# Performance work log

Measured on AMD Instinct MI355X. Metric: run time of the kernel, lower is better.

## Reference

```python
import jax, jax.numpy as jnp
import numpy as np

B_, C_, K_, STRIDE, HH = 32, 32, 3, 2, 16
H_ = 4   # h = sqrt(hh)
W_SP = 14  # input spatial width w
BATCH = 4


def setup_inputs() -> dict:
    key = jax.random.key(0)
    k1, k2, k3, k4 = jax.random.split(key, 4)
    poses = jax.random.normal(k1, (BATCH, C_, W_SP, W_SP, HH), jnp.float32)
    # variance strictly positive to keep sqrt well-behaved
    var = jax.random.uniform(k2, (BATCH, 1, C_ * W_SP * W_SP, HH), jnp.float32) * 0.9 + 0.1
    Wt = jax.random.normal(k3, (B_, K_, K_, C_, H_, H_), jnp.float32)
    # fixed gaussian noise for the reparameterized torch.normal(mu, sigma)
    noise = jax.random.normal(k4, (BATCH, B_ * K_ * K_, C_ * W_SP * W_SP, HH), jnp.float32)
    return {"poses": poses, "var": var, "Wt": Wt, "noise": noise, "out_hw": 29}


def reference(poses, var, Wt, noise, out_hw):
    b, C, w = poses.shape[0], poses.shape[1], poses.shape[2]
    Bc, K, _, _, h, _ = Wt.shape
    hh = h * h
    # inverse_EM: votes ~ Normal(mu, sqrt(var)), reparameterized
    mu = poses.reshape(b, 1, C * w * w, hh)                    # (b,1,Cww,hh)
    votes = mu + jnp.sqrt(var) * noise                          # (b,B*K*K,Cww,hh)
    # spatial flatten order of Cww is (c, j, i): k = j*w + i in the fold loop
    votes = votes.reshape(b, Bc, K, K, C, w, w, h, h)           # (b,B,ki,kj,c,j,i,h,h)
    # W_hat @ votes, then .sum over C -- fused into one einsum
    v = jnp.einsum("nklcuv,bnklcjivw->bnkljiuw", Wt, votes)     # (b,B,ki,kj,j,i,h,h)
    v = v.reshape(b, Bc, K, K, w, w, hh)                        # (b,B,ki,kj,j,i,hh)
    # fold / col2im: recon[:, :, s*i+ki, s*j+kj, :] += v[:, :, ki, kj, j, i, :]
    upd = v.transpose(0, 1, 2, 5, 3, 4, 6)                      # (b,B,ki,i,kj,j,hh)
    offs = STRIDE * jnp.arange(w)[None, :] + jnp.arange(K)[:, None]  # (K,w)
    rows = offs[:, :, None, None]                               # (K,w,1,1) -> ki,i
    cols = offs[None, None, :, :]                               # (1,1,K,w) -> kj,j
    recon = jnp.zeros((b, Bc, out_hw, out_hw, hh), poses.dtype)
    recon = recon.at[:, :, rows, cols, :].add(upd)
    return recon
```

## Files before the change

kernel.cpp:

```cpp
#include <hip/hip_runtime.h>
#include <math.h>


#define N_KL 288
#define CW2  6272
#define SPATIAL 196

__global__ void sqrt_var_kernel(const float* __restrict__ var,
                                float* __restrict__ sd, int n) {
  int idx = blockIdx.x * blockDim.x + threadIdx.x;
  if (idx < n) sd[idx] = sqrtf(var[idx]);
}

__global__ __launch_bounds__(256) void convcaps_phase1(
    const float* __restrict__ mu,
    const float* __restrict__ sd,
    const float* __restrict__ Wt,
    const float* __restrict__ noise,
    float* __restrict__ upd)
{
  __shared__ float wlds[1024];
  const int tid = threadIdx.x;
  const int BN = N_KL * SPATIAL;

  const long long S0 = (long long)blockIdx.x * 64;
  const int b0   = (int)(S0 / BN);
  const int rem0 = (int)(S0 - (long long)b0 * BN);
  const int nkl0 = rem0 / SPATIAL;
  const int nkl1 = (rem0 + 63) / SPATIAL;

  for (int f = tid; f < 1024; f += 256) {
    int sel = f >> 9;
    int rem = f & 511;
    int c = rem >> 4;
    int u = (rem >> 2) & 3;
    int v = rem & 3;
    int nk = sel ? nkl1 : nkl0;
    wlds[sel * 512 + c * 16 + v * 4 + u] = Wt[nk * 512 + rem];
  }
  __syncthreads();

  const int site_local = tid >> 2;
  const int v = tid & 3;
  const int rem = rem0 + site_local;
  const int nkl = rem / SPATIAL;
  const int s = rem - nkl * SPATIAL;
  const int sel = (nkl != nkl0) ? 1 : 0;

  const float* __restrict__ nb =
      noise + ((size_t)(b0 * N_KL + nkl) * CW2 + s) * 16 + v * 4;
  const float* __restrict__ mb = mu + ((size_t)b0 * CW2 + s) * 16 + v * 4;
  const float* __restrict__ sb = sd + ((size_t)b0 * CW2 + s) * 16 + v * 4;
  const float4* __restrict__ wf4 = (const float4*)wlds + sel * 128 + v;

  float4 acc0 = {0.f,0.f,0.f,0.f}, acc1 = {0.f,0.f,0.f,0.f};
  float4 acc2 = {0.f,0.f,0.f,0.f}, acc3 = {0.f,0.f,0.f,0.f};

  #pragma unroll 4
  for (int c = 0; c < 32; ++c) {
    const size_t off = (size_t)c * (SPATIAL * 16);
    float4 nz = *(const float4*)(nb + off);
    float4 m  = *(const float4*)(mb + off);
    float4 sv = *(const float4*)(sb + off);
    float4 w  = wf4[c * 4];
    float4 vt;
    vt.x = fmaf(sv.x, nz.x, m.x);
    vt.y = fmaf(sv.y, nz.y, m.y);
    vt.z = fmaf(sv.z, nz.z, m.z);
    vt.w = fmaf(sv.w, nz.w, m.w);
    acc0.x = fmaf(w.x, vt.x, acc0.x); acc0.y = fmaf(w.x, vt.y, acc0.y);
    acc0.z = fmaf(w.x, vt.z, acc0.z); acc0.w = fmaf(w.x, vt.w, acc0.w);
    acc1.x = fmaf(w.y, vt.x, acc1.x); acc1.y = fmaf(w.y, vt.y, acc1.y);
    acc1.z = fmaf(w.y, vt.z, acc1.z); acc1.w = fmaf(w.y, vt.w, acc1.w);
    acc2.x = fmaf(w.z, vt.x, acc2.x); acc2.y = fmaf(w.z, vt.y, acc2.y);
    acc2.z = fmaf(w.z, vt.z, acc2.z); acc2.w = fmaf(w.z, vt.w, acc2.w);
    acc3.x = fmaf(w.w, vt.x, acc3.x); acc3.y = fmaf(w.w, vt.y, acc3.y);
    acc3.z = fmaf(w.w, vt.z, acc3.z); acc3.w = fmaf(w.w, vt.w, acc3.w);
  }

  #define QRED(a) \
    a.x += __shfl_xor(a.x, 1); a.y += __shfl_xor(a.y, 1); \
    a.z += __shfl_xor(a.z, 1); a.w += __shfl_xor(a.w, 1); \
    a.x += __shfl_xor(a.x, 2); a.y += __shfl_xor(a.y, 2); \
    a.z += __shfl_xor(a.z, 2); a.w += __shfl_xor(a.w, 2);
  QRED(acc0) QRED(acc1) QRED(acc2) QRED(acc3)
  #undef QRED

  float4 r01 = (v & 1) ? acc1 : acc0;
  float4 r23 = (v & 1) ? acc3 : acc2;
  float4 myrow = (v & 2) ? r23 : r01;
  *(float4*)(upd + (S0 + site_local) * 16 + v * 4) = myrow;
}

__global__ __launch_bounds__(256) void convcaps_phase2(
    const float* __restrict__ upd, float* __restrict__ out, int total4)
{
  int t = blockIdx.x * 256 + threadIdx.x;
  if (t >= total4) return;
  int q = t & 3;
  int p = t >> 2;
  int cc = p % 29; p /= 29;
  int r  = p % 29; p /= 29;
  int n  = p & 31;
  int b  = p >> 5;

  float4 acc = {0.f, 0.f, 0.f, 0.f};
  #pragma unroll
  for (int k = 0; k < 3; ++k) {
    int ri = r - k;
    if (ri < 0 || (ri & 1)) continue;
    int i = ri >> 1;
    if (i >= 14) continue;
    #pragma unroll
    for (int l = 0; l < 3; ++l) {
      int cj = cc - l;
      if (cj < 0 || (cj & 1)) continue;
      int j = cj >> 1;
      if (j >= 14) continue;
      const float* src = upd +
          (((size_t)b * N_KL + n * 9 + k * 3 + l) * SPATIAL + j * 14 + i) * 16 + q * 4;
      float4 val = *(const float4*)src;
      acc.x += val.x; acc.y += val.y; acc.z += val.z; acc.w += val.w;
    }
  }
  *((float4*)out + t) = acc;
}

__global__ __launch_bounds__(256) void convcaps_fallback(
    const float* __restrict__ mu, const float* __restrict__ sd,
    const float* __restrict__ Wt, const float* __restrict__ noise,
    float* __restrict__ out, int sd_is_var)
{
  const int blk = blockIdx.x;
  const int b   = blk / N_KL;
  const int nkl = blk - b * N_KL;
  const int s   = threadIdx.x;
  if (s >= SPATIAL) return;
  const int j = s / 14;
  const int i = s - j * 14;
  const int n  = nkl / 9;
  const int kl = nkl - n * 9;
  const int k  = kl / 3;
  const int l  = kl - k * 3;

  const float* __restrict__ wbase = Wt + (size_t)nkl * 512;
  const float* __restrict__ nb = noise + ((size_t)blk * CW2 + s) * 16;
  const float* __restrict__ mb = mu    + ((size_t)b   * CW2 + s) * 16;
  const float* __restrict__ sb = sd    + ((size_t)b   * CW2 + s) * 16;

  float acc[4][4] = {{0,0,0,0},{0,0,0,0},{0,0,0,0},{0,0,0,0}};
  #pragma unroll 2
  for (int c = 0; c < 32; ++c) {
    const float* wc = wbase + c * 16;
    const size_t off = (size_t)c * (SPATIAL * 16);
    #pragma unroll
    for (int v = 0; v < 4; ++v) {
      float4 nz = *(const float4*)(nb + off + v * 4);
      float4 m  = *(const float4*)(mb + off + v * 4);
      float4 sv = *(const float4*)(sb + off + v * 4);
      if (sd_is_var) {
        sv.x = sqrtf(sv.x); sv.y = sqrtf(sv.y);
        sv.z = sqrtf(sv.z); sv.w = sqrtf(sv.w);
      }
      float4 vt;
      vt.x = fmaf(sv.x, nz.x, m.x);
      vt.y = fmaf(sv.y, nz.y, m.y);
      vt.z = fmaf(sv.z, nz.z, m.z);
      vt.w = fmaf(sv.w, nz.w, m.w);
      #pragma unroll
      for (int u = 0; u < 4; ++u) {
        const float wt = wc[u * 4 + v];
        acc[u][0] = fmaf(wt, vt.x, acc[u][0]);
        acc[u][1] = fmaf(wt, vt.y, acc[u][1]);
        acc[u][2] = fmaf(wt, vt.z, acc[u][2]);
        acc[u][3] = fmaf(wt, vt.w, acc[u][3]);
      }
    }
  }
  const int r  = 2 * i + k;
  const int cc = 2 * j + l;
  float* ob = out + ((((size_t)b * 32 + n) * 29 + r) * 29 + cc) * 16;
  #pragma unroll
  for (int u = 0; u < 4; ++u)
    #pragma unroll
    for (int wh = 0; wh < 4; ++wh)
      atomicAdd(ob + u * 4 + wh, acc[u][wh]);
}

extern "C" void kernel_launch(void* const* d_in, const int* in_sizes, int n_in,
                              void* d_out, int out_size, void* d_ws, size_t ws_size,
                              hipStream_t stream) {
  const float* poses = (const float*)d_in[0];
  const float* var   = (const float*)d_in[1];
  const float* Wt    = (const float*)d_in[2];
  const float* noise = (const float*)d_in[3];
  float* out = (float*)d_out;

  const int B = in_sizes[0] / (CW2 * 16);
  const int nvar = in_sizes[1];
  const size_t upd_elems = (size_t)B * N_KL * SPATIAL * 16;
  const size_t need = ((size_t)nvar + upd_elems) * sizeof(float);

  if (ws_size >= need) {
    float* sdv  = (float*)d_ws;
    float* updw = sdv + nvar;
    sqrt_var_kernel<<<(nvar + 255) / 256, 256, 0, stream>>>(var, sdv, nvar);
    const int nblk1 = (int)((size_t)B * N_KL * SPATIAL / 64);
    convcaps_phase1<<<nblk1, 256, 0, stream>>>(poses, sdv, Wt, noise, updw);
    const int total4 = out_size / 4;
    convcaps_phase2<<<(total4 + 255) / 256, 256, 0, stream>>>(updw, out, total4);
  } else {
    hipMemsetAsync(d_out, 0, (size_t)out_size * sizeof(float), stream);
    const float* sdptr;
    int sd_is_var;
    if (ws_size >= (size_t)nvar * sizeof(float)) {
      float* sdv = (float*)d_ws;
      sqrt_var_kernel<<<(nvar + 255) / 256, 256, 0, stream>>>(var, sdv, nvar);
      sdptr = sdv; sd_is_var = 0;
    } else {
      sdptr = var; sd_is_var = 1;
    }
    convcaps_fallback<<<B * N_KL, 256, 0, stream>>>(poses, sdptr, Wt, noise,
                                                    out, sd_is_var);
  }
}
```

Before: 627.3 us.

## Split mean term into separate base kernel and stream noise with nontemporal loads

Uses linearity to compute the W·mu contribution once in a new base kernel. Phase1 then only accumulates W·(sd*noise) and adds the precomputed base. Noise is read with nontemporal loads to avoid polluting caches. This adds an extra kernel launch, an extra intermediate buffer write and read, and doubles the workspace requirement, which could trigger the slow fallback path if the workspace is insufficient.

```diff
diff --git a/kernel.cpp b/kernel.cpp
--- a/kernel.cpp
+++ b/kernel.cpp
@@ -5,6 +5,8 @@
 #define N_KL 288
 #define CW2  6272
 #define SPATIAL 196
+
+typedef __attribute__((ext_vector_type(4))) float f32x4;
 
 __global__ void sqrt_var_kernel(const float* __restrict__ var,
                                 float* __restrict__ sd, int n) {
@@ -12,17 +14,15 @@
   if (idx < n) sd[idx] = sqrtf(var[idx]);
 }
 
-__global__ __launch_bounds__(256) void convcaps_phase1(
+
+__global__ __launch_bounds__(256) void convcaps_base(
     const float* __restrict__ mu,
-    const float* __restrict__ sd,
     const float* __restrict__ Wt,
-    const float* __restrict__ noise,
-    float* __restrict__ upd)
+    float* __restrict__ base)
 {
   __shared__ float wlds[1024];
   const int tid = threadIdx.x;
   const int BN = N_KL * SPATIAL;
-
   const long long S0 = (long long)blockIdx.x * 64;
   const int b0   = (int)(S0 / BN);
   const int rem0 = (int)(S0 - (long long)b0 * BN);
@@ -30,11 +30,8 @@
   const int nkl1 = (rem0 + 63) / SPATIAL;
 
   for (int f = tid; f < 1024; f += 256) {
-    int sel = f >> 9;
-    int rem = f & 511;
-    int c = rem >> 4;
-    int u = (rem >> 2) & 3;
-    int v = rem & 3;
+    int sel = f >> 9, rem = f & 511;
+    int c = rem >> 4, u = (rem >> 2) & 3, v = rem & 3;
     int nk = sel ? nkl1 : nkl0;
     wlds[sel * 512 + c * 16 + v * 4 + u] = Wt[nk * 512 + rem];
   }
@@ -47,27 +44,84 @@
   const int s = rem - nkl * SPATIAL;
   const int sel = (nkl != nkl0) ? 1 : 0;
 
+  const float* __restrict__ mb = mu + ((size_t)b0 * CW2 + s) * 16 + v * 4;
+  const f32x4* __restrict__ wf4 = (const f32x4*)wlds + sel * 128 + v;
+
+  f32x4 acc0 = 0.f, acc1 = 0.f, acc2 = 0.f, acc3 = 0.f;
+  #pragma unroll 8
+  for (int c = 0; c < 32; ++c) {
+    const size_t off = (size_t)c * (SPATIAL * 16);
+    f32x4 m = *(const f32x4*)(mb + off);
+    f32x4 w = wf4[c * 4];
+    acc0.x = fmaf(w.x, m.x, acc0.x); acc0.y = fmaf(w.x, m.y, acc0.y);
+    acc0.z = fmaf(w.x, m.z, acc0.z); acc0.w = fmaf(w.x, m.w, acc0.w);
+    acc1.x = fmaf(w.y, m.x, acc1.x); acc1.y = fmaf(w.y, m.y, acc1.y);
+    acc1.z = fmaf(w.y, m.z, acc1.z); acc1.w = fmaf(w.y, m.w, acc1.w);
+    acc2.x = fmaf(w.z, m.x, acc2.x); acc2.y = fmaf(w.z, m.y, acc2.y);
+    acc2.z = fmaf(w.z, m.z, acc2.z); acc2.w = fmaf(w.z, m.w, acc2.w);
+    acc3.x = fmaf(w.w, m.x, acc3.x); acc3.y = fmaf(w.w, m.y, acc3.y);
+    acc3.z = fmaf(w.w, m.z, acc3.z); acc3.w = fmaf(w.w, m.w, acc3.w);
+  }
+
+  #define QRED(a) \
+    a.x += __shfl_xor(a.x, 1); a.y += __shfl_xor(a.y, 1); \
+    a.z += __shfl_xor(a.z, 1); a.w += __shfl_xor(a.w, 1); \
+    a.x += __shfl_xor(a.x, 2); a.y += __shfl_xor(a.y, 2); \
+    a.z += __shfl_xor(a.z, 2); a.w += __shfl_xor(a.w, 2);
+  QRED(acc0) QRED(acc1) QRED(acc2) QRED(acc3)
+
+  f32x4 r01 = (v & 1) ? acc1 : acc0;
+  f32x4 r23 = (v & 1) ? acc3 : acc2;
+  f32x4 my  = (v & 2) ? r23 : r01;
+  *(f32x4*)(base + (S0 + site_local) * 16 + v * 4) = my;
+}
+
+__global__ __launch_bounds__(256) void convcaps_phase1(
+    const float* __restrict__ sd,
+    const float* __restrict__ Wt,
+    const float* __restrict__ noise,
+    const float* __restrict__ base,
+    float* __restrict__ upd)
+{
+  __shared__ float wlds[1024];
+  const int tid = threadIdx.x;
+  const int BN = N_KL * SPATIAL;
+  const long long S0 = (long long)blockIdx.x * 64;
+  const int b0   = (int)(S0 / BN);
+  const int rem0 = (int)(S0 - (long long)b0 * BN);
+  const int nkl0 = rem0 / SPATIAL;
+  const int nkl1 = (rem0 + 63) / SPATIAL;
+
+  for (int f = tid; f < 1024; f += 256) {
+    int sel = f >> 9, rem = f & 511;
+    int c = rem >> 4, u = (rem >> 2) & 3, v = rem & 3;
+    int nk = sel ? nkl1 : nkl0;
+    wlds[sel * 512 + c * 16 + v * 4 + u] = Wt[nk * 512 + rem];
+  }
+  __syncthreads();
+
+  const int site_local = tid >> 2;
+  const int v = tid & 3;
+  const int rem = rem0 + site_local;
+  const int nkl = rem / SPATIAL;
+  const int s = rem - nkl * SPATIAL;
+  const int sel = (nkl != nkl0) ? 1 : 0;
+
   const float* __restrict__ nb =
       noise + ((size_t)(b0 * N_KL + nkl) * CW2 + s) * 16 + v * 4;
-  const float* __restrict__ mb = mu + ((size_t)b0 * CW2 + s) * 16 + v * 4;
   const float* __restrict__ sb = sd + ((size_t)b0 * CW2 + s) * 16 + v * 4;
-  const float4* __restrict__ wf4 = (const float4*)wlds + sel * 128 + v;
-
-  float4 acc0 = {0.f,0.f,0.f,0.f}, acc1 = {0.f,0.f,0.f,0.f};
-  float4 acc2 = {0.f,0.f,0.f,0.f}, acc3 = {0.f,0.f,0.f,0.f};
-
-  #pragma unroll 4
+  const f32x4* __restrict__ wf4 = (const f32x4*)wlds + sel * 128 + v;
+
+  f32x4 acc0 = 0.f, acc1 = 0.f, acc2 = 0.f, acc3 = 0.f;
+  #pragma unroll 8
   for (int c = 0; c < 32; ++c) {
     const size_t off = (size_t)c * (SPATIAL * 16);
-    float4 nz = *(const float4*)(nb + off);
-    float4 m  = *(const float4*)(mb + off);
-    float4 sv = *(const float4*)(sb + off);
-    float4 w  = wf4[c * 4];
-    float4 vt;
-    vt.x = fmaf(sv.x, nz.x, m.x);
-    vt.y = fmaf(sv.y, nz.y, m.y);
-    vt.z = fmaf(sv.z, nz.z, m.z);
-    vt.w = fmaf(sv.w, nz.w, m.w);
+    f32x4 nz = __builtin_nontemporal_load((const f32x4*)(nb + off));
+    f32x4 sv = *(const f32x4*)(sb + off);
+    f32x4 w  = wf4[c * 4];
+    f32x4 vt;
+    vt.x = sv.x * nz.x; vt.y = sv.y * nz.y;
+    vt.z = sv.z * nz.z; vt.w = sv.w * nz.w;
     acc0.x = fmaf(w.x, vt.x, acc0.x); acc0.y = fmaf(w.x, vt.y, acc0.y);
     acc0.z = fmaf(w.x, vt.z, acc0.z); acc0.w = fmaf(w.x, vt.w, acc0.w);
     acc1.x = fmaf(w.y, vt.x, acc1.x); acc1.y = fmaf(w.y, vt.y, acc1.y);
@@ -78,18 +132,16 @@
     acc3.z = fmaf(w.w, vt.z, acc3.z); acc3.w = fmaf(w.w, vt.w, acc3.w);
   }
 
-  #define QRED(a) \
-    a.x += __shfl_xor(a.x, 1); a.y += __shfl_xor(a.y, 1); \
-    a.z += __shfl_xor(a.z, 1); a.w += __shfl_xor(a.w, 1); \
-    a.x += __shfl_xor(a.x, 2); a.y += __shfl_xor(a.y, 2); \
-    a.z += __shfl_xor(a.z, 2); a.w += __shfl_xor(a.w, 2);
   QRED(acc0) QRED(acc1) QRED(acc2) QRED(acc3)
   #undef QRED
 
-  float4 r01 = (v & 1) ? acc1 : acc0;
-  float4 r23 = (v & 1) ? acc3 : acc2;
-  float4 myrow = (v & 2) ? r23 : r01;
-  *(float4*)(upd + (S0 + site_local) * 16 + v * 4) = myrow;
+  f32x4 r01 = (v & 1) ? acc1 : acc0;
+  f32x4 r23 = (v & 1) ? acc3 : acc2;
+  f32x4 my  = (v & 2) ? r23 : r01;
+  const size_t oidx = (S0 + site_local) * 16 + v * 4;
+  f32x4 bs = *(const f32x4*)(base + oidx);
+  my.x += bs.x; my.y += bs.y; my.z += bs.z; my.w += bs.w;
+  *(f32x4*)(upd + oidx) = my;
 }
 
 __global__ __launch_bounds__(256) void convcaps_phase2(
@@ -104,7 +156,7 @@
   int n  = p & 31;
   int b  = p >> 5;
 
-  float4 acc = {0.f, 0.f, 0.f, 0.f};
+  f32x4 acc = 0.f;
   #pragma unroll
   for (int k = 0; k < 3; ++k) {
     int ri = r - k;
@@ -119,11 +171,11 @@
       if (j >= 14) continue;
       const float* src = upd +
           (((size_t)b * N_KL + n * 9 + k * 3 + l) * SPATIAL + j * 14 + i) * 16 + q * 4;
-      float4 val = *(const float4*)src;
+      f32x4 val = *(const f32x4*)src;
       acc.x += val.x; acc.y += val.y; acc.z += val.z; acc.w += val.w;
     }
   }
-  *((float4*)out + t) = acc;
+  *((f32x4*)out + t) = acc;
 }
 
 __global__ __launch_bounds__(256) void convcaps_fallback(
@@ -155,14 +207,14 @@
     const size_t off = (size_t)c * (SPATIAL * 16);
     #pragma unroll
     for (int v = 0; v < 4; ++v) {
-      float4 nz = *(const float4*)(nb + off + v * 4);
-      float4 m  = *(const float4*)(mb + off + v * 4);
-      float4 sv = *(const float4*)(sb + off + v * 4);
+      f32x4 nz = *(const f32x4*)(nb + off + v * 4);
+      f32x4 m  = *(const f32x4*)(mb + off + v * 4);
+      f32x4 sv = *(const f32x4*)(sb + off + v * 4);
       if (sd_is_var) {
         sv.x = sqrtf(sv.x); sv.y = sqrtf(sv.y);
         sv.z = sqrtf(sv.z); sv.w = sqrtf(sv.w);
       }
-      float4 vt;
+      f32x4 vt;
       vt.x = fmaf(sv.x, nz.x, m.x);
       vt.y = fmaf(sv.y, nz.y, m.y);
       vt.z = fmaf(sv.z, nz.z, m.z);
@@ -199,14 +251,16 @@
   const int B = in_sizes[0] / (CW2 * 16);
   const int nvar = in_sizes[1];
   const size_t upd_elems = (size_t)B * N_KL * SPATIAL * 16;
-  const size_t need = ((size_t)nvar + upd_elems) * sizeof(float);
+  const size_t need = ((size_t)nvar + 2 * upd_elems) * sizeof(float);
 
   if (ws_size >= need) {
-    float* sdv  = (float*)d_ws;
-    float* updw = sdv + nvar;
+    float* sdv   = (float*)d_ws;
+    float* basew = sdv + nvar;
+    float* updw  = basew + upd_elems;
     sqrt_var_kernel<<<(nvar + 255) / 256, 256, 0, stream>>>(var, sdv, nvar);
     const int nblk1 = (int)((size_t)B * N_KL * SPATIAL / 64);
-    convcaps_phase1<<<nblk1, 256, 0, stream>>>(poses, sdv, Wt, noise, updw);
+    convcaps_base<<<nblk1, 256, 0, stream>>>(poses, Wt, basew);
+    convcaps_phase1<<<nblk1, 256, 0, stream>>>(sdv, Wt, noise, basew, updw);
     const int total4 = out_size / 4;
     convcaps_phase2<<<(total4 + 255) / 256, 256, 0, stream>>>(updw, out, total4);
   } else {
```

Measured after the change: 622.7 us. No clear change (-0.7%).
